# Performance work log

Hardware: AMD Instinct MI355X
Metric: run time of the kernel (lower is better)

## Reference

```python
import jax, jax.numpy as jnp
import numpy as np

K, D, B = 2048, 50257, 256
N_CLASS = 2

def setup_inputs() -> dict:
    key = jax.random.key(0)
    k1, k2, k3 = jax.random.split(key, 3)
    # strictly positive (probability-like) entries so log() is finite
    queue_anchor = jax.random.uniform(k1, (K, D), dtype=jnp.float32, minval=1e-3, maxval=1.0)
    query = jax.random.uniform(k2, (B, D), dtype=jnp.float32, minval=1e-3, maxval=1.0)
    queue_label = jax.random.randint(k3, (K,), 0, N_CLASS, dtype=jnp.int64)
    return {"query": query, "queue_anchor": queue_anchor, "queue_label": queue_label}

def reference(query, queue_anchor, queue_label):
    # torch code: mean_d( a[:,None,:] * (log a[:,None,:] - log q) ).T  -> [B, K]
    # algebraically identical, avoiding the (K,B,D) intermediate:
    #   kl[b,k] = mean_d(a_k * log a_k) - (1/D) * sum_d a_k[d] * log q_b[d]
    d = queue_anchor.shape[1]
    self_term = jnp.mean(queue_anchor * jnp.log(queue_anchor), axis=1)        # [K]
    cross_term = jnp.einsum('kd,bd->kb', queue_anchor, jnp.log(query)) / d    # [K, B]
    kl_distance = (self_term[:, None] - cross_term).T                          # [B, K]
    # knn == 1 path: nearest anchor's label per query
    return queue_label[jnp.argmin(kl_distance, axis=1)]                        # [B]
```

## Files before the change

kernel.cpp:

```cpp
#include <hip/hip_runtime.h>


constexpr int K   = 2048;
constexpr int D   = 50257;
constexpr int B   = 256;
constexpr int BM  = 64;
constexpr int BK  = 64;
constexpr int DP  = 50320;
constexpr int NC  = 8;
constexpr float MARGIN = 4.0f;

typedef __attribute__((ext_vector_type(8))) short bf16x8;
typedef __attribute__((ext_vector_type(4))) float f32x4;
typedef __attribute__((ext_vector_type(8))) unsigned short u16x8;

__device__ inline unsigned short f2bf_rne(float f) {
    union { float f; unsigned u; } v; v.f = f;
    unsigned r = v.u + 0x7FFFu + ((v.u >> 16) & 1u);
    return (unsigned short)(r >> 16);
}

__global__ __launch_bounds__(256)
void lq_kernel(const float* __restrict__ q, unsigned short* __restrict__ lq)
{
    const int stride = gridDim.x * blockDim.x;
    const int total  = B * (DP / 4);
    for (int c = blockIdx.x * blockDim.x + threadIdx.x; c < total; c += stride) {
        const int b   = c / (DP / 4);
        const int off = (c % (DP / 4)) * 4;
        ushort4 w;
        float v0 = (off + 0 < D) ? __logf(q[(size_t)b * D + off + 0]) : 0.f;
        float v1 = (off + 1 < D) ? __logf(q[(size_t)b * D + off + 1]) : 0.f;
        float v2 = (off + 2 < D) ? __logf(q[(size_t)b * D + off + 2]) : 0.f;
        float v3 = (off + 3 < D) ? __logf(q[(size_t)b * D + off + 3]) : 0.f;
        w.x = f2bf_rne(v0); w.y = f2bf_rne(v1); w.z = f2bf_rne(v2); w.w = f2bf_rne(v3);
        *reinterpret_cast<ushort4*>(&lq[(size_t)b * DP + off]) = w;
    }
}

template<bool WSP, bool USELQ>
__global__ __launch_bounds__(512, 4)
void gemm_kernel(const float* __restrict__ anchor,
                 const float* __restrict__ query,
                 const unsigned short* __restrict__ lq,
                 float* __restrict__ outc,
                 float* __restrict__ selfp,
                 int dc, int sch)
{
    const int L   = blockIdx.x;
    const int xcd = L & 7;
    const int j   = L >> 3;
    int x, z;
    if (sch >= 8) { const int zc = sch >> 3; z = xcd * zc + (j >> 5); x = j & 31; }
    else          { const int q8 = 8 / sch;  z = xcd / q8; x = (xcd % q8) * (sch * 4) + j; }

    const int t    = threadIdx.x;
    const int k0   = x * BM;
    const int d0   = z * dc;
    const int dend = min(d0 + dc, D);

    __shared__ __align__(16) unsigned short Al[BM * 64];
    __shared__ __align__(16) unsigned short Ql[B  * 64];

    const int rowA = t >> 3;
    const int tq8  = t & 7;
    const int ar   = k0 + rowA;
    const int swA  = (rowA & 7) << 3;
    const float* Arow = anchor + (size_t)ar * D;

    const int rowQ = t >> 1;
    const int hq   = t & 1;
    const int swQ  = (rowQ & 7) << 3;
    const unsigned short* LQrow = lq    + (size_t)rowQ * DP;
    const float*          Qrow  = query + (size_t)rowQ * D;

    const int w    = t >> 6;
    const int lane = t & 63;
    const int wm   = (w >> 2) * 32;
    const int wn   = (w & 3) * 64;
    const int lrow = lane & 15;
    const int kg   = lane >> 4;

    f32x4 acc[2][4];
#pragma unroll
    for (int mt = 0; mt < 2; ++mt)
#pragma unroll
        for (int nt = 0; nt < 4; ++nt)
#pragma unroll
            for (int i = 0; i < 4; ++i) acc[mt][nt][i] = 0.f;

    float selfacc = 0.f;

    float wf[12];
    int   ph = 0;
    u16x8 qreg[4];
    float qf32[32];

    auto load_step = [&](int dt) {
        const int dbase = dt + tq8 * 8;
        if (dbase + 12 <= dend) {
            const size_t g0 = (size_t)ar * D + dbase;
            ph = (int)(g0 & 3);
            const float4* wp = reinterpret_cast<const float4*>(anchor + (g0 - ph));
            const float4 w0 = wp[0], w1 = wp[1], w2 = wp[2];
            wf[0] = w0.x; wf[1]  = w0.y; wf[2]  = w0.z; wf[3]  = w0.w;
            wf[4] = w1.x; wf[5]  = w1.y; wf[6]  = w1.z; wf[7]  = w1.w;
            wf[8] = w2.x; wf[9]  = w2.y; wf[10] = w2.z; wf[11] = w2.w;
        } else {
            ph = 0;
#pragma unroll
            for (int jj = 0; jj < 8; ++jj) {
                const int d = dbase + jj;
                wf[jj] = (d < dend) ? Arow[d] : 0.f;
            }
#pragma unroll
            for (int jj = 8; jj < 12; ++jj) wf[jj] = 0.f;
        }
        const int qb = dt + hq * 32;
        if constexpr (USELQ) {
#pragma unroll
            for (int g = 0; g < 4; ++g)
                qreg[g] = *reinterpret_cast<const u16x8*>(&LQrow[qb + 8 * g]);
        } else {
#pragma unroll
            for (int jj = 0; jj < 32; ++jj) {
                const int d = qb + jj;
                qf32[jj] = (d < dend) ? Qrow[d] : 1.f;
            }
        }
    };

    load_step(d0);

    for (int dt = d0; dt < dend; dt += BK) {
        float s1[9], av[8];
#pragma unroll
        for (int jj = 0; jj < 9; ++jj) s1[jj] = (ph & 2) ? wf[jj + 2] : wf[jj];
#pragma unroll
        for (int jj = 0; jj < 8; ++jj) av[jj] = (ph & 1) ? s1[jj + 1] : s1[jj];

        unsigned short abf[8];
#pragma unroll
        for (int jj = 0; jj < 8; ++jj) {
            if (av[jj] > 0.f) selfacc = fmaf(av[jj], __logf(av[jj]), selfacc);
            abf[jj] = f2bf_rne(av[jj]);
        }
        u16x8 qb4[4];
        if constexpr (USELQ) {
#pragma unroll
            for (int g = 0; g < 4; ++g) qb4[g] = qreg[g];
        } else {
#pragma unroll
            for (int g = 0; g < 4; ++g)
#pragma unroll
                for (int jj = 0; jj < 8; ++jj)
                    qb4[g][jj] = f2bf_rne(__logf(qf32[g * 8 + jj]));
        }

        __syncthreads();
        {
            unsigned short* a0 = &Al[rowA * 64 + ((tq8 * 8) ^ swA)];
            reinterpret_cast<ushort4*>(a0)[0] = ushort4{abf[0], abf[1], abf[2], abf[3]};
            reinterpret_cast<ushort4*>(a0)[1] = ushort4{abf[4], abf[5], abf[6], abf[7]};
#pragma unroll
            for (int g = 0; g < 4; ++g)
                *reinterpret_cast<u16x8*>(&Ql[rowQ * 64 + ((hq * 32 + 8 * g) ^ swQ)]) = qb4[g];
        }
        __syncthreads();

        if (dt + BK < dend) load_step(dt + BK);

#pragma unroll
        for (int half = 0; half < 2; ++half) {
            const int dd = half * 32;
            bf16x8 af[2], qf[4];
#pragma unroll
            for (int mt = 0; mt < 2; ++mt) {
                const int r = wm + mt * 16 + lrow;
                const int c = (dd + kg * 8) ^ ((r & 7) << 3);
                af[mt] = *reinterpret_cast<const bf16x8*>(&Al[r * 64 + c]);
            }
#pragma unroll
            for (int nt = 0; nt < 4; ++nt) {
                const int r = wn + nt * 16 + lrow;
                const int c = (dd + kg * 8) ^ ((r & 7) << 3);
                qf[nt] = *reinterpret_cast<const bf16x8*>(&Ql[r * 64 + c]);
            }
#pragma unroll
            for (int mt = 0; mt < 2; ++mt)
#pragma unroll
                for (int nt = 0; nt < 4; ++nt)
                    acc[mt][nt] = __builtin_amdgcn_mfma_f32_16x16x32_bf16(
                        af[mt], qf[nt], acc[mt][nt], 0, 0, 0);
        }
    }

#pragma unroll
    for (int mt = 0; mt < 2; ++mt)
#pragma unroll
        for (int nt = 0; nt < 4; ++nt) {
            const int kk = k0 + wm + mt * 16 + kg * 4;
            const int bb = wn + nt * 16 + lrow;
            if (WSP) {
                *reinterpret_cast<f32x4*>(&outc[((size_t)z * B + bb) * K + kk]) = acc[mt][nt];
            } else {
                float* dst = &outc[(size_t)bb * K + kk];
#pragma unroll
                for (int i = 0; i < 4; ++i) atomicAdd(&dst[i], acc[mt][nt][i]);
            }
        }

    float s = selfacc;
    s += __shfl_xor(s, 1);
    s += __shfl_xor(s, 2);
    s += __shfl_xor(s, 4);
    if (tq8 == 0) selfp[(size_t)z * K + ar] = s;
}

__global__ __launch_bounds__(256)
void selfsum_kernel(const float* __restrict__ selfp, float* __restrict__ selftot, int sch)
{
    const int k = blockIdx.x * 256 + threadIdx.x;
    float s = 0.f;
    for (int z = 0; z < sch; ++z) s += selfp[(size_t)z * K + k];
    selftot[k] = s;
}

template<bool WSP>
__global__ __launch_bounds__(256)
void topk_kernel(const float* __restrict__ outc, const float* __restrict__ selftot,
                 int* __restrict__ cand, int* __restrict__ need, int sch)
{
    const int b = blockIdx.x, t = threadIdx.x;
    float v[8];
#pragma unroll
    for (int i = 0; i < 8; ++i) {
        const int k = i * 256 + t;
        float cv = 0.f;
        if (WSP) {
            for (int z = 0; z < sch; ++z) cv += outc[((size_t)z * B + b) * K + k];
        } else {
            cv = outc[(size_t)b * K + k];
        }
        v[i] = selftot[k] - cv;
    }
    __shared__ float sv[256];
    __shared__ int   si[256];
    __shared__ float topv[2];
    for (int r = 0; r < NC; ++r) {
        float bv = 3.4e38f; int bk = K;
#pragma unroll
        for (int i = 0; i < 8; ++i) {
            const int k = i * 256 + t;
            if (v[i] < bv) { bv = v[i]; bk = k; }
        }
        sv[t] = bv; si[t] = bk;
        __syncthreads();
        for (int off = 128; off > 0; off >>= 1) {
            if (t < off) {
                if (sv[t + off] < sv[t] || (sv[t + off] == sv[t] && si[t + off] < si[t])) {
                    sv[t] = sv[t + off]; si[t] = si[t + off];
                }
            }
            __syncthreads();
        }
        const int kwin = si[0];
        if ((kwin & 255) == t) v[kwin >> 8] = 3.4e38f;
        if (t == 0) {
            cand[b * NC + r] = kwin;
            if (r < 2) topv[r] = sv[0];
        }
        __syncthreads();
    }
    if (t == 0) need[b] = (topv[1] - topv[0] < MARGIN) ? 1 : 0;
}

__global__ __launch_bounds__(512)
void rescore_kernel(const float* __restrict__ query, const float* __restrict__ anchor,
                    const int* __restrict__ cand, const int* __restrict__ need,
                    double* __restrict__ pp)
{
    const int b = blockIdx.x, h = blockIdx.y, t = threadIdx.x;
    if (!need[b]) return;
    const int dlo = h * 25129;
    const int dhi = min(D, dlo + 25129);
    int ks[NC];
#pragma unroll
    for (int c = 0; c < NC; ++c) ks[c] = cand[b * NC + c];
    const float* qrow = query + (size_t)b * D;

    double a8[NC];
#pragma unroll
    for (int c = 0; c < NC; ++c) a8[c] = 0.0;

    for (int d = dlo + t; d < dhi; d += 512) {
        const double lqv = (double)logf(qrow[d]);
#pragma unroll
        for (int c = 0; c < NC; ++c)
            a8[c] = fma((double)anchor[(size_t)ks[c] * D + d], lqv, a8[c]);
    }

    __shared__ double red[512];
    for (int c = 0; c < NC; ++c) {
        red[t] = a8[c];
        __syncthreads();
        for (int off = 256; off > 0; off >>= 1) {
            if (t < off) red[t] += red[t + off];
            __syncthreads();
        }
        if (t == 0) pp[((size_t)b * 2 + h) * NC + c] = red[0];
        __syncthreads();
    }
}

__global__ __launch_bounds__(256)
void final_kernel(const double* __restrict__ pp, const float* __restrict__ selftot,
                  const int* __restrict__ cand, const int* __restrict__ need,
                  const int* __restrict__ label, int* __restrict__ out)
{
    const int b = threadIdx.x;
    if (!need[b]) { out[b] = label[cand[b * NC]]; return; }
    float best = 3.4e38f; int bk = K;
#pragma unroll
    for (int c = 0; c < NC; ++c) {
        const int k = cand[b * NC + c];
        const double cv = pp[((size_t)b * 2 + 0) * NC + c] + pp[((size_t)b * 2 + 1) * NC + c];
        const float sc = selftot[k] - (float)cv;
        if (sc < best || (sc == best && k < bk)) { best = sc; bk = k; }
    }
    out[b] = label[bk];
}

extern "C" void kernel_launch(void* const* d_in, const int* in_sizes, int n_in,
                              void* d_out, int out_size, void* d_ws, size_t ws_size,
                              hipStream_t stream)
{
    const float* query  = (const float*)d_in[0];
    const float* anchor = (const float*)d_in[1];
    const int*   label  = (const int*)d_in[2];
    int* out = (int*)d_out;

    size_t cur = 0;
    auto alloc = [&](size_t bytes) -> void* {
        cur = (cur + 255) & ~(size_t)255;
        void* p = (char*)d_ws + cur;
        cur += bytes;
        return p;
    };

    unsigned short* lq      = (unsigned short*)alloc((size_t)B * DP * 2);
    float*          selfp   = (float*)alloc((size_t)16 * K * 4);
    float*          selftot = (float*)alloc((size_t)K * 4);
    int*            cand    = (int*)alloc((size_t)B * NC * 4);
    int*            need    = (int*)alloc((size_t)B * 4);
    double*         pp      = (double*)alloc((size_t)B * 2 * NC * 8);
    const size_t fixed_end  = cur;

    int sch = 0;
    for (int s = 16; s >= 2; s >>= 1)
        if (fixed_end + (size_t)s * B * K * 4 + 256 <= ws_size) { sch = s; break; }

    if (sch) {
        float* part = (float*)alloc((size_t)sch * B * K * 4);
        const int dc = (((D + sch - 1) / sch) + BK - 1) / BK * BK;
        lq_kernel<<<1024, 256, 0, stream>>>(query, lq);
        gemm_kernel<true, true><<<32 * sch, 512, 0, stream>>>(
            anchor, query, lq, part, selfp, dc, sch);
        selfsum_kernel<<<K / 256, 256, 0, stream>>>(selfp, selftot, sch);
        topk_kernel<true><<<B, 256, 0, stream>>>(part, selftot, cand, need, sch);
    } else if (fixed_end + (size_t)B * K * 4 + 256 <= ws_size) {
        float* cross = (float*)alloc((size_t)B * K * 4);
        const int s8 = 8;
        const int dc = (((D + s8 - 1) / s8) + BK - 1) / BK * BK;
        hipMemsetAsync(cross, 0, (size_t)B * K * sizeof(float), stream);
        lq_kernel<<<1024, 256, 0, stream>>>(query, lq);
        gemm_kernel<false, true><<<32 * s8, 512, 0, stream>>>(
            anchor, query, lq, cross, selfp, dc, s8);
        selfsum_kernel<<<K / 256, 256, 0, stream>>>(selfp, selftot, s8);
        topk_kernel<false><<<B, 256, 0, stream>>>(cross, selftot, cand, need, s8);
    } else {
        cur = 0;
        float* cross = (float*)alloc((size_t)B * K * 4);
        selfp   = (float*)alloc((size_t)16 * K * 4);
        selftot = (float*)alloc((size_t)K * 4);
        cand    = (int*)alloc((size_t)B * NC * 4);
        need    = (int*)alloc((size_t)B * 4);
        pp      = (double*)alloc((size_t)B * 2 * NC * 8);
        const int s8 = 8;
        const int dc = (((D + s8 - 1) / s8) + BK - 1) / BK * BK;
        hipMemsetAsync(cross, 0, (size_t)B * K * sizeof(float), stream);
        gemm_kernel<false, false><<<32 * s8, 512, 0, stream>>>(
            anchor, query, lq, cross, selfp, dc, s8);
        selfsum_kernel<<<K / 256, 256, 0, stream>>>(selfp, selftot, s8);
        topk_kernel<false><<<B, 256, 0, stream>>>(cross, selftot, cand, need, s8);
    }

    rescore_kernel<<<dim3(B, 2), 512, 0, stream>>>(query, anchor, cand, need, pp);
    final_kernel<<<1, 256, 0, stream>>>(pp, selftot, cand, need, label, out);
}
```

Baseline: 525.1 us.

## Fuse query log into GEMM, double-buffer LDS, and use 12-way split-D

Removes the separate lq_kernel pass and instead loads raw fp32 query values inside the GEMM, taking log and converting to bf16 on the fly. LDS is double-buffered so each iteration issues the next global loads and conversion while MFMAs run on the current buffer, which needs only one barrier per step. The split-D ladder now tries 12 chunks before 8, and the block-to-tile mapping is simplified. In exchange, the query log is recomputed by every one of the 32 K-tiles, and the larger LDS footprint may lower occupancy.

```diff
diff --git a/kernel.cpp b/kernel.cpp
--- a/kernel.cpp
+++ b/kernel.cpp
@@ -6,7 +6,6 @@
 constexpr int B   = 256;
 constexpr int BM  = 64;
 constexpr int BK  = 64;
-constexpr int DP  = 50320;
 constexpr int NC  = 8;
 constexpr float MARGIN = 4.0f;
 
@@ -20,47 +19,25 @@
     return (unsigned short)(r >> 16);
 }
 
-__global__ __launch_bounds__(256)
-void lq_kernel(const float* __restrict__ q, unsigned short* __restrict__ lq)
-{
-    const int stride = gridDim.x * blockDim.x;
-    const int total  = B * (DP / 4);
-    for (int c = blockIdx.x * blockDim.x + threadIdx.x; c < total; c += stride) {
-        const int b   = c / (DP / 4);
-        const int off = (c % (DP / 4)) * 4;
-        ushort4 w;
-        float v0 = (off + 0 < D) ? __logf(q[(size_t)b * D + off + 0]) : 0.f;
-        float v1 = (off + 1 < D) ? __logf(q[(size_t)b * D + off + 1]) : 0.f;
-        float v2 = (off + 2 < D) ? __logf(q[(size_t)b * D + off + 2]) : 0.f;
-        float v3 = (off + 3 < D) ? __logf(q[(size_t)b * D + off + 3]) : 0.f;
-        w.x = f2bf_rne(v0); w.y = f2bf_rne(v1); w.z = f2bf_rne(v2); w.w = f2bf_rne(v3);
-        *reinterpret_cast<ushort4*>(&lq[(size_t)b * DP + off]) = w;
-    }
-}
-
-template<bool WSP, bool USELQ>
+template<bool WSP>
 __global__ __launch_bounds__(512, 4)
 void gemm_kernel(const float* __restrict__ anchor,
                  const float* __restrict__ query,
-                 const unsigned short* __restrict__ lq,
                  float* __restrict__ outc,
                  float* __restrict__ selfp,
                  int dc, int sch)
 {
-    const int L   = blockIdx.x;
-    const int xcd = L & 7;
-    const int j   = L >> 3;
-    int x, z;
-    if (sch >= 8) { const int zc = sch >> 3; z = xcd * zc + (j >> 5); x = j & 31; }
-    else          { const int q8 = 8 / sch;  z = xcd / q8; x = (xcd % q8) * (sch * 4) + j; }
+    const int nb8 = gridDim.x >> 3;
+    const int g   = (blockIdx.x & 7) * nb8 + (blockIdx.x >> 3);
+    const int z   = g >> 5;
+    const int x   = g & 31;
 
     const int t    = threadIdx.x;
     const int k0   = x * BM;
     const int d0   = z * dc;
     const int dend = min(d0 + dc, D);
 
-    __shared__ __align__(16) unsigned short Al[BM * 64];
-    __shared__ __align__(16) unsigned short Ql[B  * 64];
+    __shared__ __align__(16) unsigned short lds[2][(BM + B) * 64];
 
     const int rowA = t >> 3;
     const int tq8  = t & 7;
@@ -71,8 +48,7 @@
     const int rowQ = t >> 1;
     const int hq   = t & 1;
     const int swQ  = (rowQ & 7) << 3;
-    const unsigned short* LQrow = lq    + (size_t)rowQ * DP;
-    const float*          Qrow  = query + (size_t)rowQ * D;
+    const float* Qrow = query + (size_t)rowQ * D;
 
     const int w    = t >> 6;
     const int lane = t & 63;
@@ -91,85 +67,84 @@
 
     float selfacc = 0.f;
 
-    float wf[12];
-    int   ph = 0;
-    u16x8 qreg[4];
-    float qf32[32];
+    float wfA[12]; int phA = 0;
+    float wfQ[36]; int phQ = 0;
 
     auto load_step = [&](int dt) {
         const int dbase = dt + tq8 * 8;
         if (dbase + 12 <= dend) {
             const size_t g0 = (size_t)ar * D + dbase;
-            ph = (int)(g0 & 3);
-            const float4* wp = reinterpret_cast<const float4*>(anchor + (g0 - ph));
+            phA = (int)(g0 & 3);
+            const float4* wp = reinterpret_cast<const float4*>(anchor + (g0 - phA));
             const float4 w0 = wp[0], w1 = wp[1], w2 = wp[2];
-            wf[0] = w0.x; wf[1]  = w0.y; wf[2]  = w0.z; wf[3]  = w0.w;
-            wf[4] = w1.x; wf[5]  = w1.y; wf[6]  = w1.z; wf[7]  = w1.w;
-            wf[8] = w2.x; wf[9]  = w2.y; wf[10] = w2.z; wf[11] = w2.w;
+            wfA[0] = w0.x; wfA[1]  = w0.y; wfA[2]  = w0.z; wfA[3]  = w0.w;
+            wfA[4] = w1.x; wfA[5]  = w1.y; wfA[6]  = w1.z; wfA[7]  = w1.w;
+            wfA[8] = w2.x; wfA[9]  = w2.y; wfA[10] = w2.z; wfA[11] = w2.w;
         } else {
-            ph = 0;
-#pragma unroll
-            for (int jj = 0; jj < 8; ++jj) {
-                const int d = dbase + jj;
-                wf[jj] = (d < dend) ? Arow[d] : 0.f;
-            }
-#pragma unroll
-            for (int jj = 8; jj < 12; ++jj) wf[jj] = 0.f;
+            phA = 0;
+#pragma unroll
+            for (int j = 0; j < 8; ++j) {
+                const int d = dbase + j;
+                wfA[j] = (d < dend) ? Arow[d] : 0.f;
+            }
+#pragma unroll
+            for (int j = 8; j < 12; ++j) wfA[j] = 0.f;
         }
         const int qb = dt + hq * 32;
-        if constexpr (USELQ) {
-#pragma unroll
-            for (int g = 0; g < 4; ++g)
-                qreg[g] = *reinterpret_cast<const u16x8*>(&LQrow[qb + 8 * g]);
+        if (qb + 36 <= dend) {
+            const size_t g0 = (size_t)rowQ * D + qb;
+            phQ = (int)(g0 & 3);
+            const float4* wp = reinterpret_cast<const float4*>(query + (g0 - phQ));
+#pragma unroll
+            for (int gg = 0; gg < 9; ++gg) {
+                const float4 v = wp[gg];
+                wfQ[gg * 4 + 0] = v.x; wfQ[gg * 4 + 1] = v.y;
+                wfQ[gg * 4 + 2] = v.z; wfQ[gg * 4 + 3] = v.w;
+            }
         } else {
-#pragma unroll
-            for (int jj = 0; jj < 32; ++jj) {
-                const int d = qb + jj;
-                qf32[jj] = (d < dend) ? Qrow[d] : 1.f;
-            }
+            phQ = 0;
+#pragma unroll
+            for (int j = 0; j < 32; ++j) {
+                const int d = qb + j;
+                wfQ[j] = (d < dend) ? Qrow[d] : 1.f;
+            }
+#pragma unroll
+            for (int j = 32; j < 36; ++j) wfQ[j] = 1.f;
         }
     };
 
-    load_step(d0);
-
-    for (int dt = d0; dt < dend; dt += BK) {
-        float s1[9], av[8];
-#pragma unroll
-        for (int jj = 0; jj < 9; ++jj) s1[jj] = (ph & 2) ? wf[jj + 2] : wf[jj];
-#pragma unroll
-        for (int jj = 0; jj < 8; ++jj) av[jj] = (ph & 1) ? s1[jj + 1] : s1[jj];
-
+    auto convert_write = [&](int p) {
+        float sA[9], av[8];
+#pragma unroll
+        for (int j = 0; j < 9; ++j) sA[j] = (phA & 2) ? wfA[j + 2] : wfA[j];
+#pragma unroll
+        for (int j = 0; j < 8; ++j) av[j] = (phA & 1) ? sA[j + 1] : sA[j];
         unsigned short abf[8];
 #pragma unroll
-        for (int jj = 0; jj < 8; ++jj) {
-            if (av[jj] > 0.f) selfacc = fmaf(av[jj], __logf(av[jj]), selfacc);
-            abf[jj] = f2bf_rne(av[jj]);
-        }
-        u16x8 qb4[4];
-        if constexpr (USELQ) {
-#pragma unroll
-            for (int g = 0; g < 4; ++g) qb4[g] = qreg[g];
-        } else {
-#pragma unroll
-            for (int g = 0; g < 4; ++g)
-#pragma unroll
-                for (int jj = 0; jj < 8; ++jj)
-                    qb4[g][jj] = f2bf_rne(__logf(qf32[g * 8 + jj]));
-        }
-
-        __syncthreads();
-        {
-            unsigned short* a0 = &Al[rowA * 64 + ((tq8 * 8) ^ swA)];
-            reinterpret_cast<ushort4*>(a0)[0] = ushort4{abf[0], abf[1], abf[2], abf[3]};
-            reinterpret_cast<ushort4*>(a0)[1] = ushort4{abf[4], abf[5], abf[6], abf[7]};
-#pragma unroll
-            for (int g = 0; g < 4; ++g)
-                *reinterpret_cast<u16x8*>(&Ql[rowQ * 64 + ((hq * 32 + 8 * g) ^ swQ)]) = qb4[g];
-        }
-        __syncthreads();
-
-        if (dt + BK < dend) load_step(dt + BK);
-
+        for (int j = 0; j < 8; ++j) {
+            if (av[j] > 0.f) selfacc = fmaf(av[j], __logf(av[j]), selfacc);
+            abf[j] = f2bf_rne(av[j]);
+        }
+        unsigned short* a0 = &lds[p][rowA * 64 + ((tq8 * 8) ^ swA)];
+        reinterpret_cast<ushort4*>(a0)[0] = ushort4{abf[0], abf[1], abf[2], abf[3]};
+        reinterpret_cast<ushort4*>(a0)[1] = ushort4{abf[4], abf[5], abf[6], abf[7]};
+        float sQ[34], qv[32];
+#pragma unroll
+        for (int j = 0; j < 34; ++j) sQ[j] = (phQ & 2) ? wfQ[j + 2] : wfQ[j];
+#pragma unroll
+        for (int j = 0; j < 32; ++j) qv[j] = (phQ & 1) ? sQ[j + 1] : sQ[j];
+#pragma unroll
+        for (int gg = 0; gg < 4; ++gg) {
+            u16x8 qw;
+#pragma unroll
+            for (int j = 0; j < 8; ++j)
+                qw[j] = f2bf_rne(__logf(qv[gg * 8 + j]));
+            *reinterpret_cast<u16x8*>(
+                &lds[p][(BM + rowQ) * 64 + ((hq * 32 + gg * 8) ^ swQ)]) = qw;
+        }
+    };
+
+    auto mfma_phase = [&](int p) {
 #pragma unroll
         for (int half = 0; half < 2; ++half) {
             const int dd = half * 32;
@@ -178,13 +153,13 @@
             for (int mt = 0; mt < 2; ++mt) {
                 const int r = wm + mt * 16 + lrow;
                 const int c = (dd + kg * 8) ^ ((r & 7) << 3);
-                af[mt] = *reinterpret_cast<const bf16x8*>(&Al[r * 64 + c]);
+                af[mt] = *reinterpret_cast<const bf16x8*>(&lds[p][r * 64 + c]);
             }
 #pragma unroll
             for (int nt = 0; nt < 4; ++nt) {
                 const int r = wn + nt * 16 + lrow;
                 const int c = (dd + kg * 8) ^ ((r & 7) << 3);
-                qf[nt] = *reinterpret_cast<const bf16x8*>(&Ql[r * 64 + c]);
+                qf[nt] = *reinterpret_cast<const bf16x8*>(&lds[p][(BM + r) * 64 + c]);
             }
 #pragma unroll
             for (int mt = 0; mt < 2; ++mt)
@@ -192,6 +167,24 @@
                 for (int nt = 0; nt < 4; ++nt)
                     acc[mt][nt] = __builtin_amdgcn_mfma_f32_16x16x32_bf16(
                         af[mt], qf[nt], acc[mt][nt], 0, 0, 0);
+        }
+    };
+
+    if (d0 < dend) {
+        load_step(d0);
+        convert_write(0);
+        __syncthreads();
+        int p = 0;
+        for (int dt = d0; dt < dend; dt += BK) {
+            const int nxt = dt + BK;
+            const bool more = nxt < dend;
+            if (more) load_step(nxt);
+            mfma_phase(p);
+            if (more) {
+                convert_write(p ^ 1);
+                __syncthreads();
+                p ^= 1;
+            }
         }
     }
 
@@ -348,51 +341,34 @@
         return p;
     };
 
-    unsigned short* lq      = (unsigned short*)alloc((size_t)B * DP * 2);
-    float*          selfp   = (float*)alloc((size_t)16 * K * 4);
-    float*          selftot = (float*)alloc((size_t)K * 4);
-    int*            cand    = (int*)alloc((size_t)B * NC * 4);
-    int*            need    = (int*)alloc((size_t)B * 4);
-    double*         pp      = (double*)alloc((size_t)B * 2 * NC * 8);
-    const size_t fixed_end  = cur;
+    float*  selfp   = (float*)alloc((size_t)16 * K * 4);
+    float*  selftot = (float*)alloc((size_t)K * 4);
+    int*    cand    = (int*)alloc((size_t)B * NC * 4);
+    int*    need    = (int*)alloc((size_t)B * 4);
+    double* pp      = (double*)alloc((size_t)B * 2 * NC * 8);
+    const size_t fixed_end = cur;
 
     int sch = 0;
-    for (int s = 16; s >= 2; s >>= 1)
+    const int ladder[4] = {12, 8, 4, 2};
+    for (int i = 0; i < 4; ++i) {
+        const int s = ladder[i];
         if (fixed_end + (size_t)s * B * K * 4 + 256 <= ws_size) { sch = s; break; }
+    }
 
     if (sch) {
         float* part = (float*)alloc((size_t)sch * B * K * 4);
-        const int dc = (((D + sch - 1) / sch) + BK - 1) / BK * BK;
-        lq_kernel<<<1024, 256, 0, stream>>>(query, lq);
-        gemm_kernel<true, true><<<32 * sch, 512, 0, stream>>>(
-            anchor, query, lq, part, selfp, dc, sch);
+        const int dc = (((D + sch - 1) / sch) + BK - 1) & ~(BK - 1);
+        gemm_kernel<true><<<32 * sch, 512, 0, stream>>>(anchor, query, part, selfp, dc, sch);
         selfsum_kernel<<<K / 256, 256, 0, stream>>>(selfp, selftot, sch);
         topk_kernel<true><<<B, 256, 0, stream>>>(part, selftot, cand, need, sch);
-    } else if (fixed_end + (size_t)B * K * 4 + 256 <= ws_size) {
+    } else {
         float* cross = (float*)alloc((size_t)B * K * 4);
         const int s8 = 8;
-        const int dc = (((D + s8 - 1) / s8) + BK - 1) / BK * BK;
+        const int dc = (((D + s8 - 1) / s8) + BK - 1) & ~(BK - 1);
         hipMemsetAsync(cross, 0, (size_t)B * K * sizeof(float), stream);
-        lq_kernel<<<1024, 256, 0, stream>>>(query, lq);
-        gemm_kernel<false, true><<<32 * s8, 512, 0, stream>>>(
-            anchor, query, lq, cross, selfp, dc, s8);
+        gemm_kernel<false><<<32 * s8, 512, 0, stream>>>(anchor, query, cross, selfp, dc, s8);
         selfsum_kernel<<<K / 256, 256, 0, stream>>>(selfp, selftot, s8);
         topk_kernel<false><<<B, 256, 0, stream>>>(cross, selftot, cand, need, s8);
-    } else {
-        cur = 0;
-        float* cross = (float*)alloc((size_t)B * K * 4);
-        selfp   = (float*)alloc((size_t)16 * K * 4);
-        selftot = (float*)alloc((size_t)K * 4);
-        cand    = (int*)alloc((size_t)B * NC * 4);
-        need    = (int*)alloc((size_t)B * 4);
-        pp      = (double*)alloc((size_t)B * 2 * NC * 8);
-        const int s8 = 8;
-        const int dc = (((D + s8 - 1) / s8) + BK - 1) / BK * BK;
-        hipMemsetAsync(cross, 0, (size_t)B * K * sizeof(float), stream);
-        gemm_kernel<false, false><<<32 * s8, 512, 0, stream>>>(
-            anchor, query, lq, cross, selfp, dc, s8);
-        selfsum_kernel<<<K / 256, 256, 0, stream>>>(selfp, selftot, s8);
-        topk_kernel<false><<<B, 256, 0, stream>>>(cross, selftot, cand, need, s8);
     }
 
     rescore_kernel<<<dim3(B, 2), 512, 0, stream>>>(query, anchor, cand, need, pp);
```

Result: slower. 2.093 ms (+298.5%).
